# Performance work log

Hardware: AMD Instinct MI355X
Metric: run time of the kernel (lower is better)

## Reference

```python
import jax, jax.numpy as jnp
import numpy as np

T, X_D, M_N, CHUNK, REDUCE = 2048, 2048, 64, 64, 8
M_D = X_D // REDUCE          # 256
DECAY_D = M_D // 4           # 64
H_D = X_D * 2                # factor=2
FF_D = 256 * round(int(H_D * (2.0 / 3.0)) / 256)  # 2816


def setup_inputs() -> dict:
    key = jax.random.key(0)
    ks = jax.random.split(key, 20)
    def lin(k, out_d, in_d):
        return (jax.random.normal(k, (out_d, in_d), jnp.float32) / np.sqrt(in_d).astype(np.float32))
    return {
        "xs": jax.random.normal(ks[0], (T, X_D), jnp.float32),
        "attn_q": lin(ks[1], X_D // REDUCE, X_D),
        "attn_k": lin(ks[2], X_D // REDUCE, X_D // REDUCE),
        "attn_v": lin(ks[3], X_D, X_D),
        "attn_o": lin(ks[4], X_D, X_D),
        "attn_r": lin(ks[5], X_D, X_D),
        "mem_f": lin(ks[6], M_N, X_D),
        "mem_q": lin(ks[7], M_D, X_D),
        "mem_k": lin(ks[8], M_D, M_D),
        "mem_v": lin(ks[9], M_D, X_D),
        "mem_o": lin(ks[10], X_D, M_D),
        "mem_r": lin(ks[11], X_D, X_D),
        "mem_beta": -jnp.ones((M_N, M_D), jnp.float32),
        "mem_decay": 3.0 * jnp.ones((M_N, DECAY_D), jnp.float32),
        "mem_l": jax.random.uniform(ks[12], (M_N, M_D), dtype=jnp.float32),
        "ff_in1": lin(ks[13], FF_D, X_D),
        "ff_in2": lin(ks[14], FF_D, X_D),
        "ff_out": lin(ks[15], X_D, FF_D),
        "sn1_g": jnp.sqrt(jnp.float32(X_D)),
        "sn2_g": jnp.sqrt(jnp.float32(X_D)),
    }


def _rotate_half(x):
    x1 = x[..., ::2]
    x2 = x[..., 1::2]
    return jnp.stack((-x2, x1), axis=-1).reshape(x.shape)


def _scale_norm(x, g):
    return x * (g / (jnp.linalg.norm(x, axis=-1, keepdims=True) + 1e-8))


def _attn(xs, Wq, Wk, Wv, Wo, Wr):
    n = CHUNK
    q = xs @ Wq.T                       # (T, dk)
    k = q @ Wk.T                        # k is computed from q (as in source)
    v = xs @ Wv.T                       # (T, x_d)
    c = xs.shape[0] // n
    dk = q.shape[-1]
    q = q.reshape(c, n, dk)
    k = k.reshape(c, n, dk)
    v = v.reshape(c, n, v.shape[-1])

    def with_prev(a):                   # prepend previous chunk (zero for chunk 0)
        prev = jnp.concatenate([jnp.zeros_like(a[:1]), a[:-1]], axis=0)
        return jnp.concatenate([prev, a], axis=1)   # (c, 2n, d)

    k2, v2 = with_prev(k), with_prev(v)

    # RoPE over 2n key positions; queries take the last n positions
    inv_freq = 1.0 / (10000.0 ** (jnp.arange(0, dk, 2, dtype=jnp.float32) / dk))
    ang = jnp.arange(2 * n, dtype=jnp.float32)[:, None] * inv_freq[None, :]
    sin = jnp.repeat(jnp.sin(ang), 2, axis=-1)      # (2n, dk) interleaved
    cos = jnp.repeat(jnp.cos(ang), 2, axis=-1)
    q = q * cos[None, n:] + _rotate_half(q) * sin[None, n:]
    k2 = k2 * cos[None] + _rotate_half(k2) * sin[None]

    qk = jnp.einsum('cnk,cmk->cnm', q, k2) / jnp.sqrt(jnp.float32(dk))
    allowed = jnp.arange(2 * n)[None, :] <= (jnp.arange(n)[:, None] + n)  # tril offset n
    A = jax.nn.softmax(jnp.where(allowed[None], qk, -jnp.inf), axis=-1)
    y = jnp.einsum('cnm,cmv->cnv', A, v2).reshape(xs.shape[0], -1)
    return (y @ Wo.T) * jax.nn.sigmoid(xs @ Wr.T)


def _mem(xs, Wf, Wq, Wk, Wv, Wo, Wr, beta_p, decay_p, l_p):
    v = xs @ Wv.T                                       # (T, m_d)
    f = jax.nn.sigmoid(xs @ Wf.T)[:, :, None]           # (T, m_n, 1)
    beta = jax.nn.sigmoid(beta_p)[None]                 # (1, m_n, m_d)
    gamma = jnp.concatenate(
        [jnp.ones((M_N, M_D - DECAY_D), xs.dtype), jax.nn.sigmoid(decay_p)], axis=1
    )[None]                                             # (1, m_n, m_d)
    ws = (1.0 - f * beta) * gamma                       # (T, m_n, m_d)
    fvs = f * v[:, None, :]                             # (T, m_n, m_d)

    def bin_assoc(ei, ej):
        ai, bi = ei
        aj, bj = ej
        return (aj * ai, aj * bi + bj)

    _, mems = jax.lax.associative_scan(bin_assoc, (ws, fvs), axis=0)  # (T, m_n, m_d)

    q = xs @ Wq.T                                       # (T, m_d)
    k = jnp.einsum('nmd,kd->nmk', mems, Wk) + l_p[None]
    A = jax.nn.softmax(jnp.einsum('nmk,nk->nm', k, q) / jnp.sqrt(jnp.float32(M_D)), axis=-1)
    y = jnp.einsum('nm,nmd->nd', A, mems)
    return (y @ Wo.T) * jax.nn.sigmoid(xs @ Wr.T)


def _ff(xs, W1, W2, Wo):
    return (jax.nn.silu(xs @ W1.T) * (xs @ W2.T)) @ Wo.T


def reference(xs, attn_q, attn_k, attn_v, attn_o, attn_r,
              mem_f, mem_q, mem_k, mem_v, mem_o, mem_r,
              mem_beta, mem_decay, mem_l,
              ff_in1, ff_in2, ff_out, sn1_g, sn2_g):
    xn = _scale_norm(xs, sn1_g)
    xs = (_attn(xn, attn_q, attn_k, attn_v, attn_o, attn_r)
          + _mem(xn, mem_f, mem_q, mem_k, mem_v, mem_o, mem_r, mem_beta, mem_decay, mem_l)
          + xs)
    xs = _ff(_scale_norm(xs, sn2_g), ff_in1, ff_in2, ff_out) + xs
    return xs
```

## Files before the change

kernel.cpp:

```cpp
#include <hip/hip_runtime.h>
#include <math.h>


typedef short bhalf8 __attribute__((ext_vector_type(8)));
typedef float f32x4 __attribute__((ext_vector_type(4)));

#define CC_LD 7168
#define COL_V   0
#define COL_B1  2048
#define COL_B2  4096
#define COL_QB  6144
#define COL_VM  6400
#define COL_QM  6656
#define COL_FG  6912

#define AS1 __attribute__((address_space(1)))
#define AS3 __attribute__((address_space(3)))

__device__ __forceinline__ float sigmoidf_(float x){ return 1.0f/(1.0f+expf(-x)); }

__device__ __forceinline__ unsigned short f2b(float f){
  unsigned u = __float_as_uint(f);
  unsigned r = (u + 0x7fffu + ((u>>16)&1u)) >> 16;
  return (unsigned short)r;
// ... 104 lines not shown
  int bi = blockIdx.y, bj = blockIdx.x;
  const unsigned short* Ap = A; const unsigned short* Bp = B; float* Cp = C;
  if (blockIdx.z){ Ap = A2; Bp = B2; Cp = C2; }
  int m0 = bi*128, n0 = bj*128;
  int wr = w >> 1, wc = w & 1;

  f32x4 acc[4][4];
#pragma unroll
  for (int i=0;i<4;++i)
#pragma unroll
    for (int j=0;j<4;++j){ f32x4 z = {0.f,0.f,0.f,0.f}; acc[i][j] = z; }

  const int r0 = tid >> 2;
  const int gsrc8 = (((tid&3) ^ ((tid>>3)&3)) * 8);

  auto stage = [&](int bs, int kt){
    unsigned short* db = LDSu + bs*8192;
    const unsigned short* ap0 = Ap + (size_t)(m0 + r0)*lda      + kt*32 + gsrc8;
    const unsigned short* ap1 = Ap + (size_t)(m0 + 64 + r0)*lda + kt*32 + gsrc8;
    const unsigned short* bp0 = Bp + (size_t)(n0 + r0)*K        + kt*32 + gsrc8;
    const unsigned short* bp1 = Bp + (size_t)(n0 + 64 + r0)*K   + kt*32 + gsrc8;
    __builtin_amdgcn_global_load_lds((const AS1 void*)ap0, (AS3 void*)(db + tid*8),        16, 0, 0);
    __builtin_amdgcn_global_load_lds((const AS1 void*)ap1, (AS3 void*)(db + 2048 + tid*8), 16, 0, 0);
    __builtin_amdgcn_global_load_lds((const AS1 void*)bp0, (AS3 void*)(db + 4096 + tid*8), 16, 0, 0);
    __builtin_amdgcn_global_load_lds((const AS1 void*)bp1, (AS3 void*)(db + 6144 + tid*8), 16, 0, 0);
  };

  const int nt = K >> 5;
  stage(0, 0);
  stage(1, 1);
  asm volatile("s_waitcnt vmcnt(4)" ::: "memory");
  __builtin_amdgcn_s_barrier();

  const int lr = l & 15;
  const int gsw = (((l>>4) ^ ((l>>1)&3)) * 8);
  const int aoff = (wr*64 + lr)*32 + gsw;
  const int boff = 4096 + (wc*64 + lr)*32 + gsw;

  int cur = 0;
  for (int t = 0; t < nt; ++t){
    if (t + 2 < nt) stage((t+2)%3, t+2);
    const unsigned short* Tb = LDSu + cur*8192;
    bhalf8 af[4], bfr[4];
#pragma unroll
    for (int m=0;m<4;++m) af[m]  = *(const bhalf8*)(Tb + aoff + m*512);
#pragma unroll
    for (int n=0;n<4;++n) bfr[n] = *(const bhalf8*)(Tb + boff + n*512);
    __builtin_amdgcn_s_setprio(1);
#pragma unroll
    for (int m=0;m<4;++m)
#pragma unroll
      for (int n=0;n<4;++n)
        acc[m][n] = __builtin_amdgcn_mfma_f32_16x16x32_bf16(af[m], bfr[n], acc[m][n], 0, 0, 0);
    __builtin_amdgcn_s_setprio(0);
    if (t + 1 < nt){
      if (t + 2 < nt){ asm volatile("s_waitcnt vmcnt(4)" ::: "memory"); }
      else           { asm volatile("s_waitcnt vmcnt(0)" ::: "memory"); }
      __builtin_amdgcn_s_barrier();
      cur = (cur == 2) ? 0 : cur + 1;
    }
  }

#pragma unroll
  for (int m=0;m<4;++m){
    int rowb = m0 + wr*64 + m*16 + ((l>>4)<<2);
#pragma unroll
    for (int r=0;r<4;++r){
      int row = rowb + r;
      size_t rbase = (size_t)row*ldc;
      size_t gbase = (size_t)row*gate_ld;
#pragma unroll
      for (int n=0;n<4;++n){
        int col = n0 + wc*64 + n*16 + (l&15);
        float v = acc[m][n][r];
        if (add) v += add[rbase + col];
        if (epi == 2) v *= sigmoidf_(b2f(gate[gbase + col]));
        if (epi == 3) Cb[rbase + col] = f2b(v);
        else          Cp[rbase + col] = v;
      }
    }
  }
}

__global__ __launch_bounds__(256) void k_gemm_p64(
    const unsigned short* __restrict__ A, int lda,
    const unsigned short* __restrict__ B,
    float* __restrict__ C, int K, int ldc,
    const float* __restrict__ add){
  __shared__ unsigned short LDSu[18432];
  int tid = threadIdx.x;
  int w = tid >> 6, l = tid & 63;
  int bi = blockIdx.y, bj = blockIdx.x;
  int m0 = bi*128, n0 = bj*64;
  int wr = w >> 1, wc = w & 1;

  f32x4 acc[4][2];
#pragma unroll
  for (int i=0;i<4;++i)
#pragma unroll
    for (int j=0;j<2;++j){ f32x4 z = {0.f,0.f,0.f,0.f}; acc[i][j] = z; }

  const int r0 = tid >> 2;
  const int gsrc8 = (((tid&3) ^ ((tid>>3)&3)) * 8);

  auto stage = [&](int bs, int kt){
    unsigned short* db = LDSu + bs*6144;
    const unsigned short* ap0 = A + (size_t)(m0 + r0)*lda      + kt*32 + gsrc8;
    const unsigned short* ap1 = A + (size_t)(m0 + 64 + r0)*lda + kt*32 + gsrc8;
    const unsigned short* bp0 = B + (size_t)(n0 + r0)*K        + kt*32 + gsrc8;
    __builtin_amdgcn_global_load_lds((const AS1 void*)ap0, (AS3 void*)(db + tid*8),        16, 0, 0);
    __builtin_amdgcn_global_load_lds((const AS1 void*)ap1, (AS3 void*)(db + 2048 + tid*8), 16, 0, 0);
    __builtin_amdgcn_global_load_lds((const AS1 void*)bp0, (AS3 void*)(db + 4096 + tid*8), 16, 0, 0);
  };

  const int nt = K >> 5;
  stage(0, 0);
  stage(1, 1);
  asm volatile("s_waitcnt vmcnt(3)" ::: "memory");
  __builtin_amdgcn_s_barrier();

  const int lr = l & 15;
  const int gsw = (((l>>4) ^ ((l>>1)&3)) * 8);
  const int aoff = (wr*64 + lr)*32 + gsw;
  const int boff = 4096 + (wc*32 + lr)*32 + gsw;

  int cur = 0;
  for (int t = 0; t < nt; ++t){
    if (t + 2 < nt) stage((t+2)%3, t+2);
    const unsigned short* Tb = LDSu + cur*6144;
    bhalf8 af[4], bfr[2];
#pragma unroll
    for (int m=0;m<4;++m) af[m]  = *(const bhalf8*)(Tb + aoff + m*512);
#pragma unroll
    for (int n=0;n<2;++n) bfr[n] = *(const bhalf8*)(Tb + boff + n*512);
    __builtin_amdgcn_s_setprio(1);
#pragma unroll
    for (int m=0;m<4;++m)
#pragma unroll
      for (int n=0;n<2;++n)
        acc[m][n] = __builtin_amdgcn_mfma_f32_16x16x32_bf16(af[m], bfr[n], acc[m][n], 0, 0, 0);
    __builtin_amdgcn_s_setprio(0);
    if (t + 1 < nt){
      if (t + 2 < nt){ asm volatile("s_waitcnt vmcnt(3)" ::: "memory"); }
      else           { asm volatile("s_waitcnt vmcnt(0)" ::: "memory"); }
      __builtin_amdgcn_s_barrier();
      cur = (cur == 2) ? 0 : cur + 1;
    }
  }

#pragma unroll
  for (int m=0;m<4;++m){
    int rowb = m0 + wr*64 + m*16 + ((l>>4)<<2);
#pragma unroll
    for (int r=0;r<4;++r){
      int row = rowb + r;
      size_t rbase = (size_t)row*ldc;
#pragma unroll
      for (int n=0;n<2;++n){
        int col = n0 + wc*32 + n*16 + (l&15);
        C[rbase + col] = acc[m][n][r] + add[rbase + col];
      }
    }
  }
}

__global__ __launch_bounds__(256) void k_gemm_fuse2_64(
// ... 118 lines not shown

__global__ __launch_bounds__(256) void k_gemm_silu(
    const unsigned short* __restrict__ A, int lda,
    const unsigned short* __restrict__ B,
    unsigned short* __restrict__ Cb, int K, int out_ld){
  __shared__ unsigned short LDSu[24576];
  int tid = threadIdx.x;
  int w = tid >> 6, l = tid & 63;
  int bi = blockIdx.y, bj = blockIdx.x;
  int m0 = bi*128, n0 = bj*128;
  int wr = w >> 1, wc = w & 1;

  f32x4 acc[4][4];
#pragma unroll
  for (int i=0;i<4;++i)
#pragma unroll
    for (int j=0;j<4;++j){ f32x4 z = {0.f,0.f,0.f,0.f}; acc[i][j] = z; }

  const int r0 = tid >> 2;
  const int gsrc8 = (((tid&3) ^ ((tid>>3)&3)) * 8);

  auto stage = [&](int bs, int kt){
    unsigned short* db = LDSu + bs*8192;
    const unsigned short* ap0 = A + (size_t)(m0 + r0)*lda      + kt*32 + gsrc8;
    const unsigned short* ap1 = A + (size_t)(m0 + 64 + r0)*lda + kt*32 + gsrc8;
    const unsigned short* bp0 = B + (size_t)(n0 + r0)*K        + kt*32 + gsrc8;
    const unsigned short* bp1 = B + (size_t)(n0 + 64 + r0)*K   + kt*32 + gsrc8;
    __builtin_amdgcn_global_load_lds((const AS1 void*)ap0, (AS3 void*)(db + tid*8),        16, 0, 0);
    __builtin_amdgcn_global_load_lds((const AS1 void*)ap1, (AS3 void*)(db + 2048 + tid*8), 16, 0, 0);
    __builtin_amdgcn_global_load_lds((const AS1 void*)bp0, (AS3 void*)(db + 4096 + tid*8), 16, 0, 0);
    __builtin_amdgcn_global_load_lds((const AS1 void*)bp1, (AS3 void*)(db + 6144 + tid*8), 16, 0, 0);
  };

  const int nt = K >> 5;
  stage(0, 0);
  stage(1, 1);
  asm volatile("s_waitcnt vmcnt(4)" ::: "memory");
  __builtin_amdgcn_s_barrier();

  const int lr = l & 15;
  const int gsw = (((l>>4) ^ ((l>>1)&3)) * 8);
  const int aoff = (wr*64 + lr)*32 + gsw;
  const int boff = 4096 + (wc*64 + lr)*32 + gsw;

  int cur = 0;
  for (int t = 0; t < nt; ++t){
    if (t + 2 < nt) stage((t+2)%3, t+2);
    const unsigned short* Tb = LDSu + cur*8192;
    bhalf8 af[4], bfr[4];
#pragma unroll
    for (int m=0;m<4;++m) af[m]  = *(const bhalf8*)(Tb + aoff + m*512);
#pragma unroll
    for (int n=0;n<4;++n) bfr[n] = *(const bhalf8*)(Tb + boff + n*512);
    __builtin_amdgcn_s_setprio(1);
#pragma unroll
    for (int m=0;m<4;++m)
#pragma unroll
      for (int n=0;n<4;++n)
        acc[m][n] = __builtin_amdgcn_mfma_f32_16x16x32_bf16(af[m], bfr[n], acc[m][n], 0, 0, 0);
    __builtin_amdgcn_s_setprio(0);
    if (t + 1 < nt){
      if (t + 2 < nt){ asm volatile("s_waitcnt vmcnt(4)" ::: "memory"); }
      else           { asm volatile("s_waitcnt vmcnt(0)" ::: "memory"); }
      __builtin_amdgcn_s_barrier();
      cur = (cur == 2) ? 0 : cur + 1;
    }
  }

#pragma unroll
  for (int m=0;m<4;++m){
    int rowb = m0 + wr*64 + m*16 + ((l>>4)<<2);
#pragma unroll
    for (int r=0;r<4;++r){
      int row = rowb + r;
      size_t gbase = (size_t)row*out_ld;
#pragma unroll
      for (int n=0;n<4;++n){
        int col = n0 + wc*64 + n*16 + (l&15);
        float v = acc[m][n][r];
        float o = __shfl_xor(v, 1);
        if ((l & 1) == 0)
          Cb[gbase + (col>>1)] = f2b(v*sigmoidf_(v)*o);
      }
    }
  }
}

__global__ __launch_bounds__(256) void k_attn_scores_mfma(
    const unsigned short* __restrict__ CCqb, const float* __restrict__ K0,
    const float2* __restrict__ TR, unsigned short* __restrict__ P){
  __shared__ unsigned short Ks[128*256];
  int c = blockIdx.x, tid = threadIdx.x;
  for (int it = 0; it < 16; ++it){
    int id = tid + it*256;
    int m = id >> 5;
    int cs = (id & 31) * 8;
    float v[8];
    if (c == 0 && m < 64){
#pragma unroll
      for (int u=0;u<8;++u) v[u] = 0.f;
    } else {
      int gr = (c-1)*64 + m;
      const float* kr = K0 + (size_t)gr*256 + cs;
      float4 x0 = *(const float4*)kr, x1 = *(const float4*)(kr+4);
      v[0]=x0.x; v[1]=x0.y; v[2]=x0.z; v[3]=x0.w;
      v[4]=x1.x; v[5]=x1.y; v[6]=x1.z; v[7]=x1.w;
#pragma unroll
      for (int p2=0;p2<4;++p2){
        float2 t = TR[m*128 + (cs>>1) + p2];
        float e = v[2*p2], o = v[2*p2+1];
        v[2*p2]   = e*t.x - o*t.y;
        v[2*p2+1] = o*t.x + e*t.y;
      }
    }
    unsigned short pk[8];
#pragma unroll
    for (int u=0;u<8;++u) pk[u] = f2b(v[u]);
    int byte = m*512 + ((cs*2) ^ ((m&7)<<4));
    *(bhalf8*)((char*)&Ks[0] + byte) = *(const bhalf8*)pk;
  }
  __syncthreads();

  int w = tid >> 6, l = tid & 63;
  int lr = l & 15, lkg = l >> 4;
  f32x4 acc[8];
#pragma unroll
  for (int n=0;n<8;++n){ f32x4 z = {0.f,0.f,0.f,0.f}; acc[n] = z; }

  int iq = w*16 + lr;
  const unsigned short* qbase = CCqb + (size_t)(c*64 + iq)*CC_LD;
  int pos = 64 + iq;

  for (int kt = 0; kt < 8; ++kt){
    int k0c = kt*32 + lkg*8;
    bhalf8 q8 = *(const bhalf8*)(qbase + k0c);
    float v[8];
#pragma unroll
    for (int u=0;u<8;++u) v[u] = b2f((unsigned short)(((short*)&q8)[u]));
#pragma unroll
    for (int p2=0;p2<4;++p2){
      float2 t = TR[pos*128 + (k0c>>1) + p2];
      float e = v[2*p2], o = v[2*p2+1];
      v[2*p2]   = e*t.x - o*t.y;
      v[2*p2+1] = o*t.x + e*t.y;
    }
    unsigned short pk[8];
#pragma unroll
    for (int u=0;u<8;++u) pk[u] = f2b(v[u]);
    bhalf8 af = *(const bhalf8*)pk;
#pragma unroll
    for (int n=0;n<8;++n){
      int m = n*16 + lr;
      int byte = m*512 + ((k0c*2) ^ ((m&7)<<4));
      bhalf8 bf = *(const bhalf8*)((const char*)&Ks[0] + byte);
      acc[n] = __builtin_amdgcn_mfma_f32_16x16x32_bf16(af, bf, acc[n], 0, 0, 0);
    }
  }

  int i0 = w*16 + lkg*4;
  float mx[4] = {-1e30f,-1e30f,-1e30f,-1e30f};
  float sm[4] = {0.f,0.f,0.f,0.f};
#pragma unroll
  for (int n=0;n<8;++n){
    int col = n*16 + lr;
#pragma unroll
    for (int r=0;r<4;++r){
      float vv = acc[n][r] * (1.f/16.f);
      if (col > i0 + r + 64) vv = -1e30f;
      acc[n][r] = vv;
      mx[r] = fmaxf(mx[r], vv);
    }
  }
#pragma unroll
  for (int s=1; s<16; s<<=1)
#pragma unroll
    for (int r=0;r<4;++r) mx[r] = fmaxf(mx[r], __shfl_xor(mx[r], s));
#pragma unroll
  for (int n=0;n<8;++n)
#pragma unroll
    for (int r=0;r<4;++r){
      float e = expf(acc[n][r] - mx[r]);
      acc[n][r] = e; sm[r] += e;
    }
#pragma unroll
  for (int s=1; s<16; s<<=1)
#pragma unroll
    for (int r=0;r<4;++r) sm[r] += __shfl_xor(sm[r], s);
  float rcp[4];
#pragma unroll
  for (int r=0;r<4;++r) rcp[r] = 1.f/sm[r];

  unsigned short* Pr = P + (size_t)c*8192;
#pragma unroll
  for (int n=0;n<8;++n){
    int col = n*16 + lr;
#pragma unroll
    for (int r=0;r<4;++r)
      Pr[(i0+r)*128 + col] = f2b(acc[n][r]*rcp[r]);
  }
}

__global__ __launch_bounds__(256) void k_attn_pv_mfma(
    const unsigned short* __restrict__ P, const unsigned short* __restrict__ Vb, int vld,
    unsigned short* __restrict__ Y){
  __shared__ unsigned short Vt[128*128];
  int ct = blockIdx.x, c = blockIdx.y, tid = threadIdx.x;
  {
    int k = tid >> 1;
    int ch = (tid & 1) * 64;
    if (c == 0 && k < 64){
      for (int u=0; u<64; ++u){
        int col = ch + u;
        int byte = col*256 + ((k*2) ^ ((col&7)<<4));
        *(unsigned short*)((char*)&Vt[0] + byte) = 0;
      }
    } else {
      int gr = (c-1)*64 + k;
      const unsigned short* vr = Vb + (size_t)gr*vld + ct*128 + ch;
      for (int u8=0; u8<8; ++u8){
        bhalf8 x = *(const bhalf8*)(vr + u8*8);
#pragma unroll
        for (int u=0;u<8;++u){
          int col = ch + u8*8 + u;
          int byte = col*256 + ((k*2) ^ ((col&7)<<4));
          *(unsigned short*)((char*)&Vt[0] + byte) = (unsigned short)(((short*)&x)[u]);
        }
      }
    }
  }
  __syncthreads();
  int w = tid >> 6, l = tid & 63, lr = l & 15, lkg = l >> 4;
  f32x4 acc[8];
#pragma unroll
  for (int n=0;n<8;++n){ f32x4 z = {0.f,0.f,0.f,0.f}; acc[n] = z; }
  const unsigned short* Pr = P + (size_t)c*8192;
  for (int kt=0; kt<4; ++kt){
    int kb = kt*32 + lkg*8;
    bhalf8 af = *(const bhalf8*)(Pr + (w*16 + lr)*128 + kb);
#pragma unroll
    for (int n=0;n<8;++n){
      int col = n*16 + lr;
      int byte = col*256 + ((kb*2) ^ ((col&7)<<4));
      bhalf8 bf = *(const bhalf8*)((const char*)&Vt[0] + byte);
      acc[n] = __builtin_amdgcn_mfma_f32_16x16x32_bf16(af, bf, acc[n], 0, 0, 0);
    }
  }
  int row0 = c*64 + w*16 + lkg*4;
#pragma unroll
  for (int n=0;n<8;++n){
    int col = ct*128 + n*16 + lr;
#pragma unroll
    for (int r=0;r<4;++r)
      Y[(size_t)(row0+r)*2048 + col] = f2b(acc[n][r]);
  }
}

__global__ __launch_bounds__(256) void k_scan1(const unsigned short* __restrict__ CC,
    const float* __restrict__ beta_p, const float* __restrict__ decay_p,
    float* __restrict__ CP, float* __restrict__ CQ){
  int c = blockIdx.x, mg = blockIdx.y, d = threadIdx.x;
  __shared__ float Fs[128];
  if (threadIdx.x < 128){
    int s = threadIdx.x >> 3, j = threadIdx.x & 7;
    Fs[threadIdx.x] = sigmoidf_(b2f(CC[(size_t)(c*16+s)*CC_LD + COL_FG + mg*8 + j]));
  }
  __syncthreads();
  float beta[8], gamma[8], Pa[8], Qa[8];
#pragma unroll
  for (int j=0;j<8;++j){
    int m = mg*8+j;
    beta[j]  = sigmoidf_(beta_p[m*256+d]);
    gamma[j] = (d < 192) ? 1.f : sigmoidf_(decay_p[m*64 + (d-192)]);
    Pa[j] = 1.f; Qa[j] = 0.f;
  }
  for (int s = 0; s < 16; ++s){
    float vm = b2f(CC[(size_t)(c*16+s)*CC_LD + COL_VM + d]);
#pragma unroll
    for (int j=0;j<8;++j){
      float f = Fs[s*8+j];
      float w = (1.f - f*beta[j])*gamma[j];
      Pa[j] *= w;
      Qa[j] = w*Qa[j] + f*vm;
    }
  }
#pragma unroll
  for (int j=0;j<8;++j){
    size_t idx = ((size_t)c*64 + mg*8 + j)*256 + d;
    CP[idx] = Pa[j]; CQ[idx] = Qa[j];
  }
}

__global__ __launch_bounds__(256) void k_scan2(const float* __restrict__ CP,
    const float* __restrict__ CQ, float* __restrict__ SIN){
  int m = blockIdx.x, d = threadIdx.x;
  float S = 0.f;
  for (int c = 0; c < 128; ++c){
    size_t idx = ((size_t)c*64 + m)*256 + d;
    SIN[idx] = S;
    S = CP[idx]*S + CQ[idx];
  }
}

__global__ __launch_bounds__(256) void k_scan3(const unsigned short* __restrict__ CC,
    const float* __restrict__ beta_p, const float* __restrict__ decay_p,
    const float* __restrict__ SIN, unsigned short* __restrict__ MEMS){
  int c = blockIdx.x, mg = blockIdx.y, d = threadIdx.x;
  __shared__ float Fs[128];
  if (threadIdx.x < 128){
    int s = threadIdx.x >> 3, j = threadIdx.x & 7;
    Fs[threadIdx.x] = sigmoidf_(b2f(CC[(size_t)(c*16+s)*CC_LD + COL_FG + mg*8 + j]));
  }
  __syncthreads();
  float beta[8], gamma[8], S[8];
#pragma unroll
  for (int j=0;j<8;++j){
    int m = mg*8+j;
    beta[j]  = sigmoidf_(beta_p[m*256+d]);
    gamma[j] = (d < 192) ? 1.f : sigmoidf_(decay_p[m*64 + (d-192)]);
    S[j] = SIN[((size_t)c*64 + m)*256 + d];
  }
  for (int s = 0; s < 16; ++s){
    float vm = b2f(CC[(size_t)(c*16+s)*CC_LD + COL_VM + d]);
    size_t tb = (size_t)(c*16+s)*64;
#pragma unroll
    for (int j=0;j<8;++j){
      float f = Fs[s*8+j];
      float w = (1.f - f*beta[j])*gamma[j];
      S[j] = w*S[j] + f*vm;
      MEMS[(tb + mg*8 + j)*256 + d] = f2b(S[j]);
    }
  }
}

__global__ __launch_bounds__(256) void k_memread(const unsigned short* __restrict__ MEMS,
    const float* __restrict__ QH, const unsigned short* __restrict__ QMs, int qm_ld,
    const float* __restrict__ L, unsigned short* __restrict__ YMb){
  int t = blockIdx.x, tid = threadIdx.x;
  int wave = tid >> 6, lane = tid & 63;
  __shared__ float anorm[64];
  __shared__ float red2[4][64][4];
  const unsigned short* Mt = MEMS + (size_t)t*16384;
  float4 qh4 = *(const float4*)(QH + (size_t)t*256 + lane*4);
  ushort4 qmu = *(const ushort4*)(QMs + (size_t)t*qm_ld + lane*4);
  float qm0 = b2f(qmu.x), qm1 = b2f(qmu.y), qm2 = b2f(qmu.z), qm3 = b2f(qmu.w);
  for (int mi = 0; mi < 16; ++mi){
    int m = wave*16 + mi;
    ushort4 su = *(const ushort4*)(Mt + m*256 + lane*4);
    float4 l4 = *(const float4*)(L + (size_t)m*256 + lane*4);
    float p = b2f(su.x)*qh4.x + b2f(su.y)*qh4.y + b2f(su.z)*qh4.z + b2f(su.w)*qh4.w
            + l4.x*qm0 + l4.y*qm1 + l4.z*qm2 + l4.w*qm3;
#pragma unroll
    for (int off = 32; off > 0; off >>= 1) p += __shfl_down(p, off);
    if (lane == 0) anorm[m] = p * (1.f/16.f);
  }
  __syncthreads();
  if (tid < 64){
    float v = anorm[tid];
    float mx = v;
#pragma unroll
    for (int off = 32; off > 0; off >>= 1) mx = fmaxf(mx, __shfl_xor(mx, off));
    float e = expf(v - mx);
    float s = e;
#pragma unroll
    for (int off = 32; off > 0; off >>= 1) s += __shfl_xor(s, off);
    anorm[tid] = e / s;
  }
  __syncthreads();
  int mq = tid >> 6, dq = tid & 63;
  float a0=0.f, a1=0.f, a2=0.f, a3=0.f;
#pragma unroll
  for (int mi = 0; mi < 16; ++mi){
    int m = mq*16 + mi;
    ushort4 su = *(const ushort4*)(Mt + m*256 + dq*4);
    float wgt = anorm[m];
    a0 += wgt*b2f(su.x); a1 += wgt*b2f(su.y);
    a2 += wgt*b2f(su.z); a3 += wgt*b2f(su.w);
  }
  red2[mq][dq][0]=a0; red2[mq][dq][1]=a1; red2[mq][dq][2]=a2; red2[mq][dq][3]=a3;
  __syncthreads();
  if (tid < 64){
    float r0=0.f, r1=0.f, r2=0.f, r3=0.f;
#pragma unroll
    for (int g=0; g<4; ++g){
      r0 += red2[g][tid][0]; r1 += red2[g][tid][1];
      r2 += red2[g][tid][2]; r3 += red2[g][tid][3];
    }
    ushort4 o;
    o.x = f2b(r0); o.y = f2b(r1); o.z = f2b(r2); o.w = f2b(r3);
    *(ushort4*)(YMb + (size_t)t*256 + tid*4) = o;
  }
}

extern "C" void kernel_launch(void* const* d_in, const int* in_sizes, int n_in,
                              void* d_out, int out_size, void* d_ws, size_t ws_size,
                              hipStream_t stream){
  const float* xs        = (const float*)d_in[0];
  const float* attn_q    = (const float*)d_in[1];
  const float* attn_k    = (const float*)d_in[2];
  const float* attn_v    = (const float*)d_in[3];
  const float* attn_o    = (const float*)d_in[4];
  const float* attn_r    = (const float*)d_in[5];
  const float* mem_f     = (const float*)d_in[6];
  const float* mem_q     = (const float*)d_in[7];
  const float* mem_k     = (const float*)d_in[8];
  const float* mem_v     = (const float*)d_in[9];
  const float* mem_o     = (const float*)d_in[10];
  const float* mem_r     = (const float*)d_in[11];
  const float* mem_beta  = (const float*)d_in[12];
  const float* mem_decay = (const float*)d_in[13];
  const float* mem_l     = (const float*)d_in[14];
  const float* ff1       = (const float*)d_in[15];
  const float* ff2       = (const float*)d_in[16];
  const float* ffo       = (const float*)d_in[17];
  const float* sn1       = (const float*)d_in[18];
  const float* sn2       = (const float*)d_in[19];
  float* out = (float*)d_out;
  float* W = (float*)d_ws;

  unsigned short* XNb  = (unsigned short*)(W + 0);
  unsigned short* WCAT = (unsigned short*)(W + 2097152);
  unsigned short* CCb  = (unsigned short*)(W + 9437184);
  unsigned short* AOB  = (unsigned short*)(W + 16777216);
  unsigned short* MOB  = (unsigned short*)(W + 18874368);
  unsigned short* FFW  = (unsigned short*)(W + 19136512);
  unsigned short* FFOB = (unsigned short*)(W + 24903680);
  unsigned short* AKB  = (unsigned short*)(W + 27787264);
  unsigned short* MKTB = (unsigned short*)(W + 27820032);
  unsigned short* Ybb  = (unsigned short*)(W + 27852800);
  float*          XS2  = W + 34144256;
  unsigned short* MEMSb= (unsigned short*)(W + 38338560);
  float*          CP   = W + 55115776;
  float*          CQ   = W + 57212928;
  float*          SIN  = W + 59310080;
  float2*         TRIG = (float2*)(W + 61407232);
  float*          K0   = W + 32768;
  unsigned short* P    = (unsigned short*)(W + 557056);
  float*          QH   = W + 688128;
  unsigned short* YMb  = (unsigned short*)(W + 1212416);
  unsigned short* XN2b = MEMSb;
  unsigned short* H1b  = (unsigned short*)(W + 40435712);

  dim3 blk(256);

  k_prep<<<dim3(37888), blk, 0, stream>>>(attn_v, attn_r, mem_r, attn_q, mem_v, mem_q,
      mem_f, attn_o, mem_o, ff1, ff2, ffo, attn_k, mem_k, xs, sn1,
      WCAT, AOB, MOB, FFW, FFOB, AKB, MKTB, TRIG, XNb);

  k_gemm_p<<<dim3(56, 16), blk, 0, stream>>>(XNb, 2048, WCAT, nullptr, CCb, CC_LD, 2048, CC_LD, 3,
      nullptr, nullptr, 0, nullptr, nullptr, nullptr);

  k_gemm_p<<<dim3(2, 16, 2), blk, 0, stream>>>(CCb + COL_QB, CC_LD, AKB, K0, nullptr, 256, 256, 256, 0,
      nullptr, nullptr, 0, CCb + COL_QM, MKTB, QH);

  k_attn_scores_mfma<<<dim3(32), blk, 0, stream>>>(CCb + COL_QB, K0, TRIG, P);
  k_attn_pv_mfma<<<dim3(16, 32), blk, 0, stream>>>(P, CCb + COL_V, CC_LD, Ybb);

  k_scan1<<<dim3(128, 8), blk, 0, stream>>>(CCb, mem_beta, mem_decay, CP, CQ);
  k_scan2<<<dim3(64), blk, 0, stream>>>(CP, CQ, SIN);
  k_scan3<<<dim3(128, 8), blk, 0, stream>>>(CCb, mem_beta, mem_decay, SIN, MEMSb);
  k_memread<<<dim3(2048), blk, 0, stream>>>(MEMSb, QH, CCb + COL_QM, CC_LD, mem_l, YMb);

  k_gemm_fuse2_64<<<dim3(32, 16), blk, 0, stream>>>(Ybb, AOB, YMb, MOB,
      CCb + COL_B1, CCb + COL_B2, xs, XS2);

  k_scalenorm_b<<<dim3(2048), blk, 0, stream>>>(XS2, sn2, XN2b);

  k_gemm_silu<<<dim3(44, 16), blk, 0, stream>>>(XN2b, 2048, FFW, H1b, 2048, 2816);
  k_gemm_p64<<<dim3(32, 16), blk, 0, stream>>>(H1b, 2816, FFOB, out, 2816, 2048, XS2);
}
```

Before: 391.7 us.

## Merge independent attention and memory-scan kernels into combined launches

Horizontally fuses independent stages into three combined kernels that branch on block index. The K/QH projection GEMM runs alongside scan1, attention scores alongside scan2, and attention PV alongside scan3. This cuts launch count from six to three and lets small, underfilled grids (scan2 with 64 blocks, scores with 32) overlap with other work. The cost is that each combined kernel allocates the LDS and registers of its largest branch for every block, which can lower occupancy for the lighter branches.

```diff
diff --git a/kernel.cpp b/kernel.cpp
--- a/kernel.cpp
+++ b/kernel.cpp
@@ -210,6 +210,342 @@
   }
 }
 
+__global__ __launch_bounds__(256) void k_combo1(
+    const unsigned short* __restrict__ CCb_, const unsigned short* __restrict__ AKB,
+    const unsigned short* __restrict__ MKTB, float* __restrict__ K0f, float* __restrict__ QHf,
+    const float* __restrict__ beta_p, const float* __restrict__ decay_p,
+    float* __restrict__ CP, float* __restrict__ CQ){
+  int bid = blockIdx.x, tid = threadIdx.x;
+  if (bid < 64){
+    __shared__ unsigned short LDSu[24576];
+    int w = tid >> 6, l = tid & 63;
+    int zz = bid >> 5, bi = (bid >> 1) & 15, bj = bid & 1;
+    const unsigned short* Ap = zz ? (CCb_ + COL_QM) : (CCb_ + COL_QB);
+    const unsigned short* Bp = zz ? MKTB : AKB;
+    float* Cp = zz ? QHf : K0f;
+    const int lda = CC_LD, K = 256, ldc = 256;
+    int m0 = bi*128, n0 = bj*128;
+    int wr = w >> 1, wc = w & 1;
+
+    f32x4 acc[4][4];
+#pragma unroll
+    for (int i=0;i<4;++i)
+#pragma unroll
+      for (int j=0;j<4;++j){ f32x4 z = {0.f,0.f,0.f,0.f}; acc[i][j] = z; }
+
+    const int r0 = tid >> 2;
+    const int gsrc8 = (((tid&3) ^ ((tid>>3)&3)) * 8);
+
+    auto stage = [&](int bs, int kt){
+      unsigned short* db = LDSu + bs*8192;
+      const unsigned short* ap0 = Ap + (size_t)(m0 + r0)*lda      + kt*32 + gsrc8;
+      const unsigned short* ap1 = Ap + (size_t)(m0 + 64 + r0)*lda + kt*32 + gsrc8;
+      const unsigned short* bp0 = Bp + (size_t)(n0 + r0)*K        + kt*32 + gsrc8;
+      const unsigned short* bp1 = Bp + (size_t)(n0 + 64 + r0)*K   + kt*32 + gsrc8;
+      __builtin_amdgcn_global_load_lds((const AS1 void*)ap0, (AS3 void*)(db + tid*8),        16, 0, 0);
+      __builtin_amdgcn_global_load_lds((const AS1 void*)ap1, (AS3 void*)(db + 2048 + tid*8), 16, 0, 0);
+      __builtin_amdgcn_global_load_lds((const AS1 void*)bp0, (AS3 void*)(db + 4096 + tid*8), 16, 0, 0);
+      __builtin_amdgcn_global_load_lds((const AS1 void*)bp1, (AS3 void*)(db + 6144 + tid*8), 16, 0, 0);
+    };
+
+    const int nt = 8;
+    stage(0, 0);
+    stage(1, 1);
+    asm volatile("s_waitcnt vmcnt(4)" ::: "memory");
+    __builtin_amdgcn_s_barrier();
+
+    const int lr = l & 15;
+    const int gsw = (((l>>4) ^ ((l>>1)&3)) * 8);
+    const int aoff = (wr*64 + lr)*32 + gsw;
+    const int boff = 4096 + (wc*64 + lr)*32 + gsw;
+
+    int cur = 0;
+    for (int t = 0; t < nt; ++t){
+      if (t + 2 < nt) stage((t+2)%3, t+2);
+      const unsigned short* Tb = LDSu + cur*8192;
+      bhalf8 af[4], bfr[4];
+#pragma unroll
+      for (int m=0;m<4;++m) af[m]  = *(const bhalf8*)(Tb + aoff + m*512);
+#pragma unroll
+      for (int n=0;n<4;++n) bfr[n] = *(const bhalf8*)(Tb + boff + n*512);
+      __builtin_amdgcn_s_setprio(1);
+#pragma unroll
+      for (int m=0;m<4;++m)
+#pragma unroll
+        for (int n=0;n<4;++n)
+          acc[m][n] = __builtin_amdgcn_mfma_f32_16x16x32_bf16(af[m], bfr[n], acc[m][n], 0, 0, 0);
+      __builtin_amdgcn_s_setprio(0);
+      if (t + 1 < nt){
+        if (t + 2 < nt){ asm volatile("s_waitcnt vmcnt(4)" ::: "memory"); }
+        else           { asm volatile("s_waitcnt vmcnt(0)" ::: "memory"); }
+        __builtin_amdgcn_s_barrier();
+        cur = (cur == 2) ? 0 : cur + 1;
+      }
+    }
+
+#pragma unroll
+    for (int m=0;m<4;++m){
+      int rowb = m0 + wr*64 + m*16 + ((l>>4)<<2);
+#pragma unroll
+      for (int r=0;r<4;++r){
+        size_t rbase = (size_t)(rowb + r)*ldc;
+#pragma unroll
+        for (int n=0;n<4;++n){
+          int col = n0 + wc*64 + n*16 + (l&15);
+          Cp[rbase + col] = acc[m][n][r];
+        }
+      }
+    }
+  } else {
+    int idx = bid - 64;
+    int c = idx >> 3, mg = idx & 7, d = tid;
+    __shared__ float Fs[128];
+    if (tid < 128){
+      int s = tid >> 3, j = tid & 7;
+      Fs[tid] = sigmoidf_(b2f(CCb_[(size_t)(c*16+s)*CC_LD + COL_FG + mg*8 + j]));
+    }
+    __syncthreads();
+    float beta[8], gamma[8], Pa[8], Qa[8];
+#pragma unroll
+    for (int j=0;j<8;++j){
+      int m = mg*8+j;
+      beta[j]  = sigmoidf_(beta_p[m*256+d]);
+      gamma[j] = (d < 192) ? 1.f : sigmoidf_(decay_p[m*64 + (d-192)]);
+      Pa[j] = 1.f; Qa[j] = 0.f;
+    }
+    for (int s = 0; s < 16; ++s){
+      float vm = b2f(CCb_[(size_t)(c*16+s)*CC_LD + COL_VM + d]);
+#pragma unroll
+      for (int j=0;j<8;++j){
+        float f = Fs[s*8+j];
+        float w = (1.f - f*beta[j])*gamma[j];
+        Pa[j] *= w;
+        Qa[j] = w*Qa[j] + f*vm;
+      }
+    }
+#pragma unroll
+    for (int j=0;j<8;++j){
+      size_t oidx = ((size_t)c*64 + mg*8 + j)*256 + d;
+      CP[oidx] = Pa[j]; CQ[oidx] = Qa[j];
+    }
+  }
+}
+
+__global__ __launch_bounds__(256) void k_combo2(
+    const unsigned short* __restrict__ CCqb, const float* __restrict__ K0,
+    const float2* __restrict__ TR, unsigned short* __restrict__ P,
+    const float* __restrict__ CP, const float* __restrict__ CQ, float* __restrict__ SIN){
+  int bid = blockIdx.x, tid = threadIdx.x;
+  if (bid < 32){
+    __shared__ unsigned short Ks[128*256];
+    int c = bid;
+    for (int it = 0; it < 16; ++it){
+      int id = tid + it*256;
+      int m = id >> 5;
+      int cs = (id & 31) * 8;
+      float v[8];
+      if (c == 0 && m < 64){
+#pragma unroll
+        for (int u=0;u<8;++u) v[u] = 0.f;
+      } else {
+        int gr = (c-1)*64 + m;
+        const float* kr = K0 + (size_t)gr*256 + cs;
+        float4 x0 = *(const float4*)kr, x1 = *(const float4*)(kr+4);
+        v[0]=x0.x; v[1]=x0.y; v[2]=x0.z; v[3]=x0.w;
+        v[4]=x1.x; v[5]=x1.y; v[6]=x1.z; v[7]=x1.w;
+#pragma unroll
+        for (int p2=0;p2<4;++p2){
+          float2 t = TR[m*128 + (cs>>1) + p2];
+          float e = v[2*p2], o = v[2*p2+1];
+          v[2*p2]   = e*t.x - o*t.y;
+          v[2*p2+1] = o*t.x + e*t.y;
+        }
+      }
+      unsigned short pk[8];
+#pragma unroll
+      for (int u=0;u<8;++u) pk[u] = f2b(v[u]);
+      int byte = m*512 + ((cs*2) ^ ((m&7)<<4));
+      *(bhalf8*)((char*)&Ks[0] + byte) = *(const bhalf8*)pk;
+    }
+    __syncthreads();
+
+    int w = tid >> 6, l = tid & 63;
+    int lr = l & 15, lkg = l >> 4;
+    f32x4 acc[8];
+#pragma unroll
+    for (int n=0;n<8;++n){ f32x4 z = {0.f,0.f,0.f,0.f}; acc[n] = z; }
+
+    int iq = w*16 + lr;
+    const unsigned short* qbase = CCqb + (size_t)(c*64 + iq)*CC_LD;
+    int pos = 64 + iq;
+
+    for (int kt = 0; kt < 8; ++kt){
+      int k0c = kt*32 + lkg*8;
+      bhalf8 q8 = *(const bhalf8*)(qbase + k0c);
+      float v[8];
+#pragma unroll
+      for (int u=0;u<8;++u) v[u] = b2f((unsigned short)(((short*)&q8)[u]));
+#pragma unroll
+      for (int p2=0;p2<4;++p2){
+        float2 t = TR[pos*128 + (k0c>>1) + p2];
+        float e = v[2*p2], o = v[2*p2+1];
+        v[2*p2]   = e*t.x - o*t.y;
+        v[2*p2+1] = o*t.x + e*t.y;
+      }
+      unsigned short pk[8];
+#pragma unroll
+      for (int u=0;u<8;++u) pk[u] = f2b(v[u]);
+      bhalf8 af = *(const bhalf8*)pk;
+#pragma unroll
+      for (int n=0;n<8;++n){
+        int m = n*16 + lr;
+        int byte = m*512 + ((k0c*2) ^ ((m&7)<<4));
+        bhalf8 bf = *(const bhalf8*)((const char*)&Ks[0] + byte);
+        acc[n] = __builtin_amdgcn_mfma_f32_16x16x32_bf16(af, bf, acc[n], 0, 0, 0);
+      }
+    }
+
+    int i0 = w*16 + lkg*4;
+    float mx[4] = {-1e30f,-1e30f,-1e30f,-1e30f};
+    float sm[4] = {0.f,0.f,0.f,0.f};
+#pragma unroll
+    for (int n=0;n<8;++n){
+      int col = n*16 + lr;
+#pragma unroll
+      for (int r=0;r<4;++r){
+        float vv = acc[n][r] * (1.f/16.f);
+        if (col > i0 + r + 64) vv = -1e30f;
+        acc[n][r] = vv;
+        mx[r] = fmaxf(mx[r], vv);
+      }
+    }
+#pragma unroll
+    for (int s=1; s<16; s<<=1)
+#pragma unroll
+      for (int r=0;r<4;++r) mx[r] = fmaxf(mx[r], __shfl_xor(mx[r], s));
+#pragma unroll
+    for (int n=0;n<8;++n)
+#pragma unroll
+      for (int r=0;r<4;++r){
+        float e = expf(acc[n][r] - mx[r]);
+        acc[n][r] = e; sm[r] += e;
+      }
+#pragma unroll
+    for (int s=1; s<16; s<<=1)
+#pragma unroll
+      for (int r=0;r<4;++r) sm[r] += __shfl_xor(sm[r], s);
+    float rcp[4];
+#pragma unroll
+    for (int r=0;r<4;++r) rcp[r] = 1.f/sm[r];
+
+    unsigned short* Pr = P + (size_t)c*8192;
+#pragma unroll
+    for (int n=0;n<8;++n){
+      int col = n*16 + lr;
+#pragma unroll
+      for (int r=0;r<4;++r)
+        Pr[(i0+r)*128 + col] = f2b(acc[n][r]*rcp[r]);
+    }
+  } else {
+    int m = bid - 32, d = tid;
+    float S = 0.f;
+    for (int c = 0; c < 128; ++c){
+      size_t idx = ((size_t)c*64 + m)*256 + d;
+      SIN[idx] = S;
+      S = CP[idx]*S + CQ[idx];
+    }
+  }
+}
+
+__global__ __launch_bounds__(256) void k_combo3(
+    const unsigned short* __restrict__ P, const unsigned short* __restrict__ Vb, int vld,
+    unsigned short* __restrict__ Y,
+    const unsigned short* __restrict__ CC, const float* __restrict__ beta_p,
+    const float* __restrict__ decay_p, const float* __restrict__ SIN,
+    unsigned short* __restrict__ MEMS){
+  int bid = blockIdx.x, tid = threadIdx.x;
+  if (bid < 512){
+    __shared__ unsigned short Vt[128*128];
+    int ct = bid & 15, c = bid >> 4;
+    {
+      int k = tid >> 1;
+      int ch = (tid & 1) * 64;
+      if (c == 0 && k < 64){
+        for (int u=0; u<64; ++u){
+          int col = ch + u;
+          int byte = col*256 + ((k*2) ^ ((col&7)<<4));
+          *(unsigned short*)((char*)&Vt[0] + byte) = 0;
+        }
+      } else {
+        int gr = (c-1)*64 + k;
+        const unsigned short* vr = Vb + (size_t)gr*vld + ct*128 + ch;
+        for (int u8=0; u8<8; ++u8){
+          bhalf8 x = *(const bhalf8*)(vr + u8*8);
+#pragma unroll
+          for (int u=0;u<8;++u){
+            int col = ch + u8*8 + u;
+            int byte = col*256 + ((k*2) ^ ((col&7)<<4));
+            *(unsigned short*)((char*)&Vt[0] + byte) = (unsigned short)(((short*)&x)[u]);
+          }
+        }
+      }
+    }
+    __syncthreads();
+    int w = tid >> 6, l = tid & 63, lr = l & 15, lkg = l >> 4;
+    f32x4 acc[8];
+#pragma unroll
+    for (int n=0;n<8;++n){ f32x4 z = {0.f,0.f,0.f,0.f}; acc[n] = z; }
+    const unsigned short* Pr = P + (size_t)c*8192;
+    for (int kt=0; kt<4; ++kt){
+      int kb = kt*32 + lkg*8;
+      bhalf8 af = *(const bhalf8*)(Pr + (w*16 + lr)*128 + kb);
+#pragma unroll
+      for (int n=0;n<8;++n){
+        int col = n*16 + lr;
+        int byte = col*256 + ((kb*2) ^ ((col&7)<<4));
+        bhalf8 bf = *(const bhalf8*)((const char*)&Vt[0] + byte);
+        acc[n] = __builtin_amdgcn_mfma_f32_16x16x32_bf16(af, bf, acc[n], 0, 0, 0);
+      }
+    }
+    int row0 = c*64 + w*16 + lkg*4;
+#pragma unroll
+    for (int n=0;n<8;++n){
+      int col = ct*128 + n*16 + lr;
+#pragma unroll
+      for (int r=0;r<4;++r)
+        Y[(size_t)(row0+r)*2048 + col] = f2b(acc[n][r]);
+    }
+  } else {
+    int idx = bid - 512;
+    int c = idx >> 3, mg = idx & 7, d = tid;
+    __shared__ float Fs[128];
+    if (tid < 128){
+      int s = tid >> 3, j = tid & 7;
+      Fs[tid] = sigmoidf_(b2f(CC[(size_t)(c*16+s)*CC_LD + COL_FG + mg*8 + j]));
+    }
+    __syncthreads();
+    float beta[8], gamma[8], S[8];
+#pragma unroll
+    for (int j=0;j<8;++j){
+      int m = mg*8+j;
+      beta[j]  = sigmoidf_(beta_p[m*256+d]);
+      gamma[j] = (d < 192) ? 1.f : sigmoidf_(decay_p[m*64 + (d-192)]);
+      S[j] = SIN[((size_t)c*64 + m)*256 + d];
+    }
+    for (int s = 0; s < 16; ++s){
+      float vm = b2f(CC[(size_t)(c*16+s)*CC_LD + COL_VM + d]);
+      size_t tb = (size_t)(c*16+s)*64;
+#pragma unroll
+      for (int j=0;j<8;++j){
+        float f = Fs[s*8+j];
+        float w = (1.f - f*beta[j])*gamma[j];
+        S[j] = w*S[j] + f*vm;
+        MEMS[(tb + mg*8 + j)*256 + d] = f2b(S[j]);
+      }
+    }
+  }
+}
+
 __global__ __launch_bounds__(256) void k_gemm_p64(
     const unsigned short* __restrict__ A, int lda,
     const unsigned short* __restrict__ B,
@@ -494,252 +830,6 @@
         if ((l & 1) == 0)
           Cb[gbase + (col>>1)] = f2b(v*sigmoidf_(v)*o);
       }
-    }
-  }
-}
-
-__global__ __launch_bounds__(256) void k_attn_scores_mfma(
-    const unsigned short* __restrict__ CCqb, const float* __restrict__ K0,
-    const float2* __restrict__ TR, unsigned short* __restrict__ P){
-  __shared__ unsigned short Ks[128*256];
-  int c = blockIdx.x, tid = threadIdx.x;
-  for (int it = 0; it < 16; ++it){
-    int id = tid + it*256;
-    int m = id >> 5;
-    int cs = (id & 31) * 8;
-    float v[8];
-    if (c == 0 && m < 64){
-#pragma unroll
-      for (int u=0;u<8;++u) v[u] = 0.f;
-    } else {
-      int gr = (c-1)*64 + m;
-      const float* kr = K0 + (size_t)gr*256 + cs;
-      float4 x0 = *(const float4*)kr, x1 = *(const float4*)(kr+4);
-      v[0]=x0.x; v[1]=x0.y; v[2]=x0.z; v[3]=x0.w;
-      v[4]=x1.x; v[5]=x1.y; v[6]=x1.z; v[7]=x1.w;
-#pragma unroll
-      for (int p2=0;p2<4;++p2){
-        float2 t = TR[m*128 + (cs>>1) + p2];
-        float e = v[2*p2], o = v[2*p2+1];
-        v[2*p2]   = e*t.x - o*t.y;
-        v[2*p2+1] = o*t.x + e*t.y;
-      }
-    }
-    unsigned short pk[8];
-#pragma unroll
-    for (int u=0;u<8;++u) pk[u] = f2b(v[u]);
-    int byte = m*512 + ((cs*2) ^ ((m&7)<<4));
-    *(bhalf8*)((char*)&Ks[0] + byte) = *(const bhalf8*)pk;
-  }
-  __syncthreads();
-
-  int w = tid >> 6, l = tid & 63;
-  int lr = l & 15, lkg = l >> 4;
-  f32x4 acc[8];
-#pragma unroll
-  for (int n=0;n<8;++n){ f32x4 z = {0.f,0.f,0.f,0.f}; acc[n] = z; }
-
-  int iq = w*16 + lr;
-  const unsigned short* qbase = CCqb + (size_t)(c*64 + iq)*CC_LD;
-  int pos = 64 + iq;
-
-  for (int kt = 0; kt < 8; ++kt){
-    int k0c = kt*32 + lkg*8;
-    bhalf8 q8 = *(const bhalf8*)(qbase + k0c);
-    float v[8];
-#pragma unroll
-    for (int u=0;u<8;++u) v[u] = b2f((unsigned short)(((short*)&q8)[u]));
-#pragma unroll
-    for (int p2=0;p2<4;++p2){
-      float2 t = TR[pos*128 + (k0c>>1) + p2];
-      float e = v[2*p2], o = v[2*p2+1];
-      v[2*p2]   = e*t.x - o*t.y;
-      v[2*p2+1] = o*t.x + e*t.y;
-    }
-    unsigned short pk[8];
-#pragma unroll
-    for (int u=0;u<8;++u) pk[u] = f2b(v[u]);
-    bhalf8 af = *(const bhalf8*)pk;
-#pragma unroll
-    for (int n=0;n<8;++n){
-      int m = n*16 + lr;
-      int byte = m*512 + ((k0c*2) ^ ((m&7)<<4));
-      bhalf8 bf = *(const bhalf8*)((const char*)&Ks[0] + byte);
-      acc[n] = __builtin_amdgcn_mfma_f32_16x16x32_bf16(af, bf, acc[n], 0, 0, 0);
-    }
-  }
-
-  int i0 = w*16 + lkg*4;
-  float mx[4] = {-1e30f,-1e30f,-1e30f,-1e30f};
-  float sm[4] = {0.f,0.f,0.f,0.f};
-#pragma unroll
-  for (int n=0;n<8;++n){
-    int col = n*16 + lr;
-#pragma unroll
-    for (int r=0;r<4;++r){
-      float vv = acc[n][r] * (1.f/16.f);
-      if (col > i0 + r + 64) vv = -1e30f;
-      acc[n][r] = vv;
-      mx[r] = fmaxf(mx[r], vv);
-    }
-  }
-#pragma unroll
-  for (int s=1; s<16; s<<=1)
-#pragma unroll
-    for (int r=0;r<4;++r) mx[r] = fmaxf(mx[r], __shfl_xor(mx[r], s));
-#pragma unroll
-  for (int n=0;n<8;++n)
-#pragma unroll
-    for (int r=0;r<4;++r){
-      float e = expf(acc[n][r] - mx[r]);
-      acc[n][r] = e; sm[r] += e;
-    }
-#pragma unroll
-  for (int s=1; s<16; s<<=1)
-#pragma unroll
-    for (int r=0;r<4;++r) sm[r] += __shfl_xor(sm[r], s);
-  float rcp[4];
-#pragma unroll
-  for (int r=0;r<4;++r) rcp[r] = 1.f/sm[r];
-
-  unsigned short* Pr = P + (size_t)c*8192;
-#pragma unroll
-  for (int n=0;n<8;++n){
-    int col = n*16 + lr;
-#pragma unroll
-    for (int r=0;r<4;++r)
-      Pr[(i0+r)*128 + col] = f2b(acc[n][r]*rcp[r]);
-  }
-}
-
-__global__ __launch_bounds__(256) void k_attn_pv_mfma(
-    const unsigned short* __restrict__ P, const unsigned short* __restrict__ Vb, int vld,
-    unsigned short* __restrict__ Y){
-  __shared__ unsigned short Vt[128*128];
-  int ct = blockIdx.x, c = blockIdx.y, tid = threadIdx.x;
-  {
-    int k = tid >> 1;
-    int ch = (tid & 1) * 64;
-    if (c == 0 && k < 64){
-      for (int u=0; u<64; ++u){
-        int col = ch + u;
-        int byte = col*256 + ((k*2) ^ ((col&7)<<4));
-        *(unsigned short*)((char*)&Vt[0] + byte) = 0;
-      }
-    } else {
-      int gr = (c-1)*64 + k;
-      const unsigned short* vr = Vb + (size_t)gr*vld + ct*128 + ch;
-      for (int u8=0; u8<8; ++u8){
-        bhalf8 x = *(const bhalf8*)(vr + u8*8);
-#pragma unroll
-        for (int u=0;u<8;++u){
-          int col = ch + u8*8 + u;
-          int byte = col*256 + ((k*2) ^ ((col&7)<<4));
-          *(unsigned short*)((char*)&Vt[0] + byte) = (unsigned short)(((short*)&x)[u]);
-        }
-      }
-    }
-  }
-  __syncthreads();
-  int w = tid >> 6, l = tid & 63, lr = l & 15, lkg = l >> 4;
-  f32x4 acc[8];
-#pragma unroll
-  for (int n=0;n<8;++n){ f32x4 z = {0.f,0.f,0.f,0.f}; acc[n] = z; }
-  const unsigned short* Pr = P + (size_t)c*8192;
-  for (int kt=0; kt<4; ++kt){
-    int kb = kt*32 + lkg*8;
-    bhalf8 af = *(const bhalf8*)(Pr + (w*16 + lr)*128 + kb);
-#pragma unroll
-    for (int n=0;n<8;++n){
-      int col = n*16 + lr;
-      int byte = col*256 + ((kb*2) ^ ((col&7)<<4));
-      bhalf8 bf = *(const bhalf8*)((const char*)&Vt[0] + byte);
-      acc[n] = __builtin_amdgcn_mfma_f32_16x16x32_bf16(af, bf, acc[n], 0, 0, 0);
-    }
-  }
-  int row0 = c*64 + w*16 + lkg*4;
-#pragma unroll
-  for (int n=0;n<8;++n){
-    int col = ct*128 + n*16 + lr;
-#pragma unroll
-    for (int r=0;r<4;++r)
-      Y[(size_t)(row0+r)*2048 + col] = f2b(acc[n][r]);
-  }
-}
-
-__global__ __launch_bounds__(256) void k_scan1(const unsigned short* __restrict__ CC,
-    const float* __restrict__ beta_p, const float* __restrict__ decay_p,
-    float* __restrict__ CP, float* __restrict__ CQ){
-  int c = blockIdx.x, mg = blockIdx.y, d = threadIdx.x;
-  __shared__ float Fs[128];
-  if (threadIdx.x < 128){
-    int s = threadIdx.x >> 3, j = threadIdx.x & 7;
-    Fs[threadIdx.x] = sigmoidf_(b2f(CC[(size_t)(c*16+s)*CC_LD + COL_FG + mg*8 + j]));
-  }
-  __syncthreads();
-  float beta[8], gamma[8], Pa[8], Qa[8];
-#pragma unroll
-  for (int j=0;j<8;++j){
-    int m = mg*8+j;
-    beta[j]  = sigmoidf_(beta_p[m*256+d]);
-    gamma[j] = (d < 192) ? 1.f : sigmoidf_(decay_p[m*64 + (d-192)]);
-    Pa[j] = 1.f; Qa[j] = 0.f;
-  }
-  for (int s = 0; s < 16; ++s){
-    float vm = b2f(CC[(size_t)(c*16+s)*CC_LD + COL_VM + d]);
-#pragma unroll
-    for (int j=0;j<8;++j){
-      float f = Fs[s*8+j];
-      float w = (1.f - f*beta[j])*gamma[j];
-      Pa[j] *= w;
-      Qa[j] = w*Qa[j] + f*vm;
-    }
-  }
-#pragma unroll
-  for (int j=0;j<8;++j){
-    size_t idx = ((size_t)c*64 + mg*8 + j)*256 + d;
-    CP[idx] = Pa[j]; CQ[idx] = Qa[j];
-  }
-}
-
-__global__ __launch_bounds__(256) void k_scan2(const float* __restrict__ CP,
-    const float* __restrict__ CQ, float* __restrict__ SIN){
-  int m = blockIdx.x, d = threadIdx.x;
-  float S = 0.f;
-  for (int c = 0; c < 128; ++c){
-    size_t idx = ((size_t)c*64 + m)*256 + d;
-    SIN[idx] = S;
-    S = CP[idx]*S + CQ[idx];
-  }
-}
-
-__global__ __launch_bounds__(256) void k_scan3(const unsigned short* __restrict__ CC,
-    const float* __restrict__ beta_p, const float* __restrict__ decay_p,
-    const float* __restrict__ SIN, unsigned short* __restrict__ MEMS){
-  int c = blockIdx.x, mg = blockIdx.y, d = threadIdx.x;
-  __shared__ float Fs[128];
-  if (threadIdx.x < 128){
-    int s = threadIdx.x >> 3, j = threadIdx.x & 7;
-    Fs[threadIdx.x] = sigmoidf_(b2f(CC[(size_t)(c*16+s)*CC_LD + COL_FG + mg*8 + j]));
-  }
-  __syncthreads();
-  float beta[8], gamma[8], S[8];
-#pragma unroll
-  for (int j=0;j<8;++j){
-    int m = mg*8+j;
-    beta[j]  = sigmoidf_(beta_p[m*256+d]);
-    gamma[j] = (d < 192) ? 1.f : sigmoidf_(decay_p[m*64 + (d-192)]);
-    S[j] = SIN[((size_t)c*64 + m)*256 + d];
-  }
-  for (int s = 0; s < 16; ++s){
-    float vm = b2f(CC[(size_t)(c*16+s)*CC_LD + COL_VM + d]);
-    size_t tb = (size_t)(c*16+s)*64;
-#pragma unroll
-    for (int j=0;j<8;++j){
-      float f = Fs[s*8+j];
-      float w = (1.f - f*beta[j])*gamma[j];
-      S[j] = w*S[j] + f*vm;
-      MEMS[(tb + mg*8 + j)*256 + d] = f2b(S[j]);
     }
   }
 }
@@ -861,15 +951,14 @@
   k_gemm_p<<<dim3(56, 16), blk, 0, stream>>>(XNb, 2048, WCAT, nullptr, CCb, CC_LD, 2048, CC_LD, 3,
       nullptr, nullptr, 0, nullptr, nullptr, nullptr);
 
-  k_gemm_p<<<dim3(2, 16, 2), blk, 0, stream>>>(CCb + COL_QB, CC_LD, AKB, K0, nullptr, 256, 256, 256, 0,
-      nullptr, nullptr, 0, CCb + COL_QM, MKTB, QH);
-
-  k_attn_scores_mfma<<<dim3(32), blk, 0, stream>>>(CCb + COL_QB, K0, TRIG, P);
-  k_attn_pv_mfma<<<dim3(16, 32), blk, 0, stream>>>(P, CCb + COL_V, CC_LD, Ybb);
-
-  k_scan1<<<dim3(128, 8), blk, 0, stream>>>(CCb, mem_beta, mem_decay, CP, CQ);
-  k_scan2<<<dim3(64), blk, 0, stream>>>(CP, CQ, SIN);
-  k_scan3<<<dim3(128, 8), blk, 0, stream>>>(CCb, mem_beta, mem_decay, SIN, MEMSb);
+  k_combo1<<<dim3(1088), blk, 0, stream>>>(CCb, AKB, MKTB, K0, QH,
+      mem_beta, mem_decay, CP, CQ);
+
+  k_combo2<<<dim3(96), blk, 0, stream>>>(CCb + COL_QB, K0, TRIG, P, CP, CQ, SIN);
+
+  k_combo3<<<dim3(1536), blk, 0, stream>>>(P, CCb + COL_V, CC_LD, Ybb,
+      CCb, mem_beta, mem_decay, SIN, MEMSb);
+
   k_memread<<<dim3(2048), blk, 0, stream>>>(MEMSb, QH, CCb + COL_QM, CC_LD, mem_l, YMb);
 
   k_gemm_fuse2_64<<<dim3(32, 16), blk, 0, stream>>>(Ybb, AOB, YMb, MOB,
```

Measured after the change: 375.0 us, median of 2. 1.04x faster.
